# Optimization experiments

Hardware: AMD Instinct MI355X
Metric: run time of the kernel (lower is better)

Reference implementation:

```python
import jax, jax.numpy as jnp
import numpy as np

N = 200000   # num_nodes
D = 64       # embedding_dims
B = 4096     # batch of target nodes (batched per-edge processing)
K = 128      # padded in-neighbor count per target
W = 20       # window_size (history deque length)
H = 128      # hidden_size


def setup_inputs() -> dict:
    key = jax.random.key(0)
    ks = jax.random.split(key, 14)
    return {
        "adj_time": jax.random.uniform(ks[0], (N,), jnp.float32),          # last-seen times in [0,1)
        "gc": jax.random.uniform(ks[1], (N,), jnp.float32),                 # per-node centrality scalar (dict_gc)
        "cur_time": jnp.ones((1,), jnp.float32),                            # current event time (>= all stored times)
        "neigh_mask": jnp.ones((B, K), jnp.float32),                        # 1 = valid neighbor slot
        "hist_feat": jax.random.normal(ks[2], (B, W, 2 * D), jnp.float32),  # feature_dict[...]['feature'] deque
        "hist_time": jax.random.uniform(ks[3], (B, W), jnp.float32),        # feature_dict[...]['time'] deque
        "t2v_w": jax.random.normal(ks[4], (D,), jnp.float32),               # Time2Vec('cos') weights
        "t2v_b": jax.random.normal(ks[5], (D,), jnp.float32),
        "node_w": jax.random.normal(ks[6], (D,), jnp.float32),              # linear_node: Linear(1, D)
        "node_b": jax.random.normal(ks[7], (D,), jnp.float32),
        "att_w": jax.random.normal(ks[8], (2 * D,), jnp.float32),           # Attention: score = cat(a,b) @ w + b
        "att_b": jax.random.normal(ks[9], (1,), jnp.float32),
        "weight": jax.random.normal(ks[10], (H, 4 * D), jnp.float32) * 0.05,
        "targets": jax.random.randint(ks[11], (B,), 0, N),
        "neigh_idx": jax.random.randint(ks[12], (B, K), 0, N),
    }


def reference(adj_time, gc, cur_time, neigh_mask, hist_feat, hist_time,
              t2v_w, t2v_b, node_w, node_b, att_w, att_b, weight,
              targets, neigh_idx):
    t = cur_time[0]

    def node_encoding(idx):
        # Time2Vec('cos'): first channel linear, rest cos(w*dt+b)
        dt = jnp.abs(t - adj_time[idx])[..., None]            # [..., 1]
        phase = t2v_w * dt + t2v_b                            # [..., D]
        tv = jnp.concatenate([phase[..., :1], jnp.cos(phase[..., 1:])], axis=-1)
        feat = jax.nn.relu(tv + gc[idx][..., None] * node_w + node_b)
        # F.normalize (L2 over feature dim)
        return feat / jnp.maximum(jnp.linalg.norm(feat, axis=-1, keepdims=True), 1e-12)

    tgt_feat = node_encoding(targets)       # [B, D]
    ngh_feat = node_encoding(neigh_idx)     # [B, K, D]

    # Decayer(2, 'log'): time_score = 1 / (2 * log(e + dt))
    time_score = 1.0 / (2.0 * jnp.log(jnp.e + (t - adj_time[neigh_idx])))   # [B, K]
    # Attention score between target and each neighbor encoding
    att = (tgt_feat @ att_w[:D])[:, None] \
        + jnp.einsum("bkd,d->bk", ngh_feat, att_w[D:]) + att_b[0]           # [B, K]
    score = jax.nn.leaky_relu(time_score + att, 0.01) * neigh_mask          # [B, K]
    neigh_agg = jnp.einsum("bk,bkd->bd", score, ngh_feat)                   # [B, D]

    combined = jnp.concatenate([tgt_feat, neigh_agg], axis=-1)              # [B, 2D]

    # History aggregation with Decayer(2, 'rev'): w = 1 / (2 * (1 + dt))
    hist_w = 1.0 / (2.0 * (1.0 + (t - hist_time)))                          # [B, W]
    hist_agg = jnp.einsum("bw,bwd->bd", hist_w, hist_feat)                  # [B, 2D]

    feat4 = jnp.concatenate([hist_agg, combined], axis=-1)                  # [B, 4D]
    return jax.nn.relu(feat4 @ weight.T)                                    # [B, H]
```

## Files before the change

### kernel.cpp

```cpp
#include <hip/hip_runtime.h>
#include <math.h>

#define NN 200000
#define DD 64
#define BB 4096
#define KK 128
#define WW 20
#define HH 128
#define TPB 512
#define RPB 4
#define TSTRIDE 260

__device__ __forceinline__ float fast_rcp(float x) { return __builtin_amdgcn_rcpf(x); }
__device__ __forceinline__ float fast_rsq(float x) { return __builtin_amdgcn_rsqf(x); }
__device__ __forceinline__ float readlane_f(float v, int l) {
    return __builtin_bit_cast(float, __builtin_amdgcn_readlane(__builtin_bit_cast(int, v), l));
}

__global__ __launch_bounds__(512, 8) void fused(
    const float* __restrict__ adj_time, const float* __restrict__ gc,
    const float* __restrict__ cur_time, const float* __restrict__ neigh_mask,
    const float* __restrict__ hist_feat, const float* __restrict__ hist_time,
    const float* __restrict__ t2v_w, const float* __restrict__ t2v_b,
    const float* __restrict__ node_w, const float* __restrict__ node_b,
    const float* __restrict__ att_w, const float* __restrict__ att_b,
    const float* __restrict__ weight,
    const int* __restrict__ targets, const int* __restrict__ neigh_idx,
    float* __restrict__ out)
{
    const int b0   = blockIdx.x * RPB;
    const int tid  = threadIdx.x;
    const int lane = tid & 63;
    const int wv   = tid >> 6;
    const int r_   = tid >> 7;
    const int d_   = tid & 127;

    __shared__ float hws[RPB][WW];
    __shared__ float stL[RPB];
    __shared__ float tile[RPB * TSTRIDE];
    __shared__ float aggp[8][64];

    const float t = cur_time[0];

    float m_k, g, dt, ts_k;
    {
        int idx = neigh_idx[b0 * KK + tid];
        m_k     = neigh_mask[b0 * KK + tid];
        float a = adj_time[idx];
        g       = gc[idx];
        dt      = fabsf(t - a);
        ts_k    = fast_rcp(2.0f * __logf(2.71828182845904523536f + (t - a)));
    }
    if (tid < RPB * WW) {
        int r = tid / WW, w = tid - r * WW;
        hws[r][w] = fast_rcp(2.0f * (1.0f + (t - hist_time[(b0 + r) * WW + w])));
    }
    if (wv < RPB) {
        int   tg  = targets[b0 + wv];
        float dtT = fabsf(t - adj_time[tg]);
        float gT  = gc[tg];
        float ph  = fmaf(t2v_w[lane], dtT, t2v_b[lane]);
        float tv_ = (lane == 0) ? ph : __cosf(ph);
        float f   = fmaxf(tv_ + fmaf(gT, node_w[lane], node_b[lane]), 0.f);
        float ss  = f * f;
#pragma unroll
        for (int off = 32; off; off >>= 1) ss += __shfl_xor(ss, off, 64);
        float invn = fast_rsq(fmaxf(ss, 1e-24f));
        float tfn  = f * invn;
        float sdt  = tfn * att_w[lane];
#pragma unroll
        for (int off = 32; off; off >>= 1) sdt += __shfl_xor(sdt, off, 64);
        if (lane == 0) stL[wv] = sdt;
        tile[wv * TSTRIDE + 128 + lane] = tfn;
    }
    __syncthreads();

    float wk;
    {
        float ph0 = fmaf(t2v_w[0], dt, t2v_b[0]);
        float f0  = fmaxf(ph0 + fmaf(g, node_w[0], node_b[0]), 0.f);
        float s2  = f0 * f0;
        float sd  = f0 * att_w[64];
#pragma unroll 9
        for (int d = 1; d < 64; ++d) {
            float ph = fmaf(t2v_w[d], dt, t2v_b[d]);
            float f  = fmaxf(__cosf(ph) + fmaf(g, node_w[d], node_b[d]), 0.f);
            s2 = fmaf(f, f, s2);
            sd = fmaf(f, att_w[64 + d], sd);
        }
        float invn = fast_rsq(fmaxf(s2, 1e-24f));
        float sc   = ts_k + stL[r_] + sd * invn + att_b[0];
        sc = (sc > 0.f) ? sc : 0.01f * sc;
        wk = sc * m_k * invn;
    }

    {
        const float* hf = hist_feat + (size_t)(b0 + r_) * WW * 128 + d_;
        float s = 0.f;
#pragma unroll
        for (int w = 0; w < WW; ++w) s = fmaf(hws[r_][w], hf[w * 128], s);
        tile[r_ * TSTRIDE + d_] = s;
    }

    {
        float pw = t2v_w[lane], pb = t2v_b[lane];
        float nw = node_w[lane], nb2 = node_b[lane];
        float acc = 0.f;
#pragma unroll
        for (int j = 0; j < 64; ++j) {
            float dtj = readlane_f(dt, j);
            float gj  = readlane_f(g,  j);
            float wkj = readlane_f(wk, j);
            float ph  = fmaf(pw, dtj, pb);
            float cv  = __cosf(ph);
            float tv_ = (lane == 0) ? ph : cv;
            float f   = fmaxf(tv_ + fmaf(gj, nw, nb2), 0.f);
            acc = fmaf(wkj, f, acc);
        }
        aggp[wv][lane] = acc;
    }
    __syncthreads();

    if (!(wv & 1))
        tile[(wv >> 1) * TSTRIDE + 192 + lane] = aggp[wv][lane] + aggp[wv | 1][lane];
    __syncthreads();

    {
        const int h = wv * 16 + (lane >> 2);
        const int r = lane & 3;
        const float4* wrow = (const float4*)(weight + (size_t)h * 256);
        const float*  tb   = tile + r * TSTRIDE;
        float acc = 0.f;
#pragma unroll 8
        for (int j = 0; j < 64; ++j) {
            float4 w4 = wrow[j];
            float4 f4 = *(const float4*)(tb + 4 * j);
            acc += w4.x * f4.x + w4.y * f4.y + w4.z * f4.z + w4.w * f4.w;
        }
        out[(size_t)(b0 + r) * 128 + h] = fmaxf(acc, 0.f);
    }
}

extern "C" void kernel_launch(void* const* d_in, const int* in_sizes, int n_in,
                              void* d_out, int out_size, void* d_ws, size_t ws_size,
                              hipStream_t stream) {
    const float* adj_time  = (const float*)d_in[0];
    const float* gc        = (const float*)d_in[1];
    const float* cur_time  = (const float*)d_in[2];
    const float* neigh_mask= (const float*)d_in[3];
    const float* hist_feat = (const float*)d_in[4];
    const float* hist_time = (const float*)d_in[5];
    const float* t2v_w     = (const float*)d_in[6];
    const float* t2v_b     = (const float*)d_in[7];
    const float* node_w    = (const float*)d_in[8];
    const float* node_b    = (const float*)d_in[9];
    const float* att_w     = (const float*)d_in[10];
    const float* att_b     = (const float*)d_in[11];
    const float* weight    = (const float*)d_in[12];
    const int*   targets   = (const int*)d_in[13];
    const int*   neigh_idx = (const int*)d_in[14];

    float* out = (float*)d_out;

    fused<<<BB / RPB, TPB, 0, stream>>>(adj_time, gc, cur_time, neigh_mask,
                                        hist_feat, hist_time, t2v_w, t2v_b,
                                        node_w, node_b, att_w, att_b, weight,
                                        targets, neigh_idx, out);
}
```

Measured before the change: 137.5 us.

## Precompute per-node encodings in a pre-pass kernel and gather them in the fused kernel

Adds a first kernel that computes the normalized Time2Vec node encoding, its attention dot product and its time decay once for every one of the N nodes, writing them to workspace. The main kernel then gathers these precomputed rows by neighbor and target index instead of recomputing cosines per neighbor slot, where each slot was previously encoded twice. This trades the repeated transcendental work for a large workspace write over all nodes plus random-row gathers of 256-byte encodings, and it relies on the workspace being big enough.

After: 175.2 us. 1.27x slower.

```diff
diff --git a/kernel.cpp b/kernel.cpp
--- a/kernel.cpp
+++ b/kernel.cpp
@@ -17,15 +17,49 @@
     return __builtin_bit_cast(float, __builtin_amdgcn_readlane(__builtin_bit_cast(int, v), l));
 }
 
+__global__ __launch_bounds__(256) void k0_nodes(
+    const float* __restrict__ adj_time, const float* __restrict__ gc,
+    const float* __restrict__ cur_time,
+    const float* __restrict__ t2v_w, const float* __restrict__ t2v_b,
+    const float* __restrict__ node_w, const float* __restrict__ node_b,
+    const float* __restrict__ att_w,
+    float* __restrict__ fn, float2* __restrict__ snt)
+{
+    const int tid  = threadIdx.x;
+    const int lane = tid & 63;
+    const int node = blockIdx.x * 4 + (tid >> 6);
+
+    const float t  = cur_time[0];
+    const float at = adj_time[node];
+    const float g  = gc[node];
+    const float dt = fabsf(t - at);
+
+    float ph = fmaf(t2v_w[lane], dt, t2v_b[lane]);
+    float tv = (lane == 0) ? ph : __cosf(ph);
+    float f  = fmaxf(tv + fmaf(g, node_w[lane], node_b[lane]), 0.f);
+
+    float s2 = f * f;
+    float sd = f * att_w[64 + lane];
+#pragma unroll
+    for (int off = 32; off; off >>= 1) {
+        s2 += __shfl_xor(s2, off, 64);
+        sd += __shfl_xor(sd, off, 64);
+    }
+    float invn = fast_rsq(fmaxf(s2, 1e-24f));
+    fn[(size_t)node * 64 + lane] = f * invn;
+    if (lane == 0) {
+        float ts = fast_rcp(2.0f * __logf(2.71828182845904523536f + (t - at)));
+        snt[node] = make_float2(sd * invn, ts);
+    }
+}
+
 __global__ __launch_bounds__(512, 8) void fused(
-    const float* __restrict__ adj_time, const float* __restrict__ gc,
     const float* __restrict__ cur_time, const float* __restrict__ neigh_mask,
     const float* __restrict__ hist_feat, const float* __restrict__ hist_time,
-    const float* __restrict__ t2v_w, const float* __restrict__ t2v_b,
-    const float* __restrict__ node_w, const float* __restrict__ node_b,
     const float* __restrict__ att_w, const float* __restrict__ att_b,
     const float* __restrict__ weight,
     const int* __restrict__ targets, const int* __restrict__ neigh_idx,
+    const float* __restrict__ fn, const float2* __restrict__ snt,
     float* __restrict__ out)
 {
     const int b0   = blockIdx.x * RPB;
@@ -42,32 +76,18 @@
 
     const float t = cur_time[0];
 
-    float m_k, g, dt, ts_k;
-    {
-        int idx = neigh_idx[b0 * KK + tid];
-        m_k     = neigh_mask[b0 * KK + tid];
-        float a = adj_time[idx];
-        g       = gc[idx];
-        dt      = fabsf(t - a);
-        ts_k    = fast_rcp(2.0f * __logf(2.71828182845904523536f + (t - a)));
-    }
+    int    idx = neigh_idx[b0 * KK + tid];
+    float  m_k = neigh_mask[b0 * KK + tid];
+    float2 s   = snt[idx];
+
     if (tid < RPB * WW) {
         int r = tid / WW, w = tid - r * WW;
         hws[r][w] = fast_rcp(2.0f * (1.0f + (t - hist_time[(b0 + r) * WW + w])));
     }
     if (wv < RPB) {
         int   tg  = targets[b0 + wv];
-        float dtT = fabsf(t - adj_time[tg]);
-        float gT  = gc[tg];
-        float ph  = fmaf(t2v_w[lane], dtT, t2v_b[lane]);
-        float tv_ = (lane == 0) ? ph : __cosf(ph);
-        float f   = fmaxf(tv_ + fmaf(gT, node_w[lane], node_b[lane]), 0.f);
-        float ss  = f * f;
-#pragma unroll
-        for (int off = 32; off; off >>= 1) ss += __shfl_xor(ss, off, 64);
-        float invn = fast_rsq(fmaxf(ss, 1e-24f));
-        float tfn  = f * invn;
-        float sdt  = tfn * att_w[lane];
+        float tfn = fn[(size_t)tg * 64 + lane];
+        float sdt = tfn * att_w[lane];
 #pragma unroll
         for (int off = 32; off; off >>= 1) sdt += __shfl_xor(sdt, off, 64);
         if (lane == 0) stL[wv] = sdt;
@@ -77,45 +97,27 @@
 
     float wk;
     {
-        float ph0 = fmaf(t2v_w[0], dt, t2v_b[0]);
-        float f0  = fmaxf(ph0 + fmaf(g, node_w[0], node_b[0]), 0.f);
-        float s2  = f0 * f0;
-        float sd  = f0 * att_w[64];
-#pragma unroll 9
-        for (int d = 1; d < 64; ++d) {
-            float ph = fmaf(t2v_w[d], dt, t2v_b[d]);
-            float f  = fmaxf(__cosf(ph) + fmaf(g, node_w[d], node_b[d]), 0.f);
-            s2 = fmaf(f, f, s2);
-            sd = fmaf(f, att_w[64 + d], sd);
-        }
-        float invn = fast_rsq(fmaxf(s2, 1e-24f));
-        float sc   = ts_k + stL[r_] + sd * invn + att_b[0];
+        float sc = s.y + stL[r_] + s.x + att_b[0];
         sc = (sc > 0.f) ? sc : 0.01f * sc;
-        wk = sc * m_k * invn;
+        wk = sc * m_k;
     }
 
     {
         const float* hf = hist_feat + (size_t)(b0 + r_) * WW * 128 + d_;
-        float s = 0.f;
+        float hs = 0.f;
 #pragma unroll
-        for (int w = 0; w < WW; ++w) s = fmaf(hws[r_][w], hf[w * 128], s);
-        tile[r_ * TSTRIDE + d_] = s;
+        for (int w = 0; w < WW; ++w) hs = fmaf(hws[r_][w], hf[w * 128], hs);
+        tile[r_ * TSTRIDE + d_] = hs;
     }
 
     {
-        float pw = t2v_w[lane], pb = t2v_b[lane];
-        float nw = node_w[lane], nb2 = node_b[lane];
         float acc = 0.f;
 #pragma unroll
         for (int j = 0; j < 64; ++j) {
-            float dtj = readlane_f(dt, j);
-            float gj  = readlane_f(g,  j);
+            int   ij  = __builtin_amdgcn_readlane(idx, j);
             float wkj = readlane_f(wk, j);
-            float ph  = fmaf(pw, dtj, pb);
-            float cv  = __cosf(ph);
-            float tv_ = (lane == 0) ? ph : cv;
-            float f   = fmaxf(tv_ + fmaf(gj, nw, nb2), 0.f);
-            acc = fmaf(wkj, f, acc);
+            float fv  = fn[(size_t)ij * 64 + lane];
+            acc = fmaf(wkj, fv, acc);
         }
         aggp[wv][lane] = acc;
     }
@@ -162,8 +164,15 @@
 
     float* out = (float*)d_out;
 
-    fused<<<BB / RPB, TPB, 0, stream>>>(adj_time, gc, cur_time, neigh_mask,
-                                        hist_feat, hist_time, t2v_w, t2v_b,
-                                        node_w, node_b, att_w, att_b, weight,
-                                        targets, neigh_idx, out);
+    float*  fn  = (float*)d_ws;
+    float2* snt = (float2*)((char*)d_ws + (size_t)NN * 64 * sizeof(float));
+
+    k0_nodes<<<NN / 4, 256, 0, stream>>>(adj_time, gc, cur_time,
+                                         t2v_w, t2v_b, node_w, node_b, att_w,
+                                         fn, snt);
+
+    fused<<<BB / RPB, TPB, 0, stream>>>(cur_time, neigh_mask,
+                                        hist_feat, hist_time,
+                                        att_w, att_b, weight,
+                                        targets, neigh_idx, fn, snt, out);
 }
```
